# Performance work log

Measured on AMD Instinct MI355X. Metric: run time of the kernel, lower is better.

## Reference

```python
import jax, jax.numpy as jnp
import numpy as np

HIDDEN = 2048
HEADS = 16
HEAD_DIM = HIDDEN // HEADS
B, S = 4, 2048
NEG_INF = float('-inf')


def setup_inputs() -> dict:
    key = jax.random.key(0)
    ks = jax.random.split(key, 9)
    x = jax.random.normal(ks[0], (B, S, HIDDEN), dtype=jnp.float32)
    # causal mask: 0 on/below diagonal, -inf above (matches masked_fill(mask == -inf))
    causal = jnp.tril(jnp.ones((S, S), dtype=bool))
    mask = jnp.where(causal, 0.0, NEG_INF).astype(jnp.float32)[None, None]
    sc = 1.0 / np.sqrt(HIDDEN)
    Wq = jax.random.normal(ks[1], (HIDDEN, HIDDEN), jnp.float32) * sc
    Wk = jax.random.normal(ks[2], (HIDDEN, HIDDEN), jnp.float32) * sc
    Wv = jax.random.normal(ks[3], (HIDDEN, HIDDEN), jnp.float32) * sc
    Wo = jax.random.normal(ks[4], (HIDDEN, HIDDEN), jnp.float32) * sc
    bq = jax.random.normal(ks[5], (HIDDEN,), jnp.float32) * 0.02
    bk = jax.random.normal(ks[6], (HIDDEN,), jnp.float32) * 0.02
    bv = jax.random.normal(ks[7], (HIDDEN,), jnp.float32) * 0.02
    bo = jax.random.normal(ks[8], (HIDDEN,), jnp.float32) * 0.02
    return {"x": x, "mask": mask, "Wq": Wq, "bq": bq, "Wk": Wk, "bk": bk,
            "Wv": Wv, "bv": bv, "Wo": Wo, "bo": bo}


def reference(x, mask, Wq, bq, Wk, bk, Wv, bv, Wo, bo):
    Bsz, Slen, H = x.shape
    scale = jnp.float32(HEAD_DIM) ** 0.5
    # torch Linear: y = x @ W.T + b
    def proj(W, b):
        y = jnp.einsum('bsh,oh->bso', x, W) + b
        return y.reshape(Bsz, Slen, HEADS, HEAD_DIM).transpose(0, 2, 1, 3)  # [B,H,S,D]
    q = proj(Wq, bq)
    k = proj(Wk, bk)
    v = proj(Wv, bv)
    scores = jnp.einsum('bhqd,bhkd->bhqk', q, k) / scale
    scores = jnp.where(mask == NEG_INF, NEG_INF, scores)
    attn = jax.nn.softmax(scores, axis=-1)  # dropout is identity in eval
    ctx = jnp.einsum('bhqk,bhkd->bhqd', attn, v)
    ctx = ctx.transpose(0, 2, 1, 3).reshape(Bsz, Slen, H)
    return jnp.einsum('bsh,oh->bso', ctx, Wo) + bo
```

## Files before the change

### kernel.cpp

```cpp
#include <hip/hip_runtime.h>
#include <hip/hip_bf16.h>

#define HID 2048
#define NH 16
#define HD 128
#define SQ 2048
#define NB 4

typedef __attribute__((ext_vector_type(8))) short short8;
typedef __attribute__((ext_vector_type(4))) float f32x4;

__device__ __forceinline__ unsigned short f2bf(float f) {
  unsigned int u = __float_as_uint(f);
  u += 0x7fffu + ((u >> 16) & 1u);
  return (unsigned short)(u >> 16);
}
__device__ __forceinline__ unsigned int pkbf(float a, float b) {
  unsigned int ua = __float_as_uint(a) + 0x8000u;
  unsigned int ub = __float_as_uint(b) + 0x8000u;
  return (ua >> 16) | (ub & 0xffff0000u);
}
__device__ __forceinline__ f32x4 mfma16(short8 a, short8 b, f32x4 c) {
  return __builtin_amdgcn_mfma_f32_16x16x32_bf16(a, b, c, 0, 0, 0);
}
__device__ __forceinline__ void dma16(const void* g, void* l) {
  __builtin_amdgcn_global_load_lds(
      (__attribute__((address_space(1))) void*)(uintptr_t)g,
      (__attribute__((address_space(3))) void*)(uintptr_t)l, 16, 0, 0);
}
__device__ __forceinline__ void wgbar() {
  asm volatile("" ::: "memory");
  __builtin_amdgcn_s_barrier();
  asm volatile("" ::: "memory");
}

__global__ __launch_bounds__(256)
void cvt_bf16(const float* __restrict__ X, const float* __restrict__ Wq,
              const float* __restrict__ Wk, const float* __restrict__ Wv,
              const float* __restrict__ Wo, unsigned short* __restrict__ xbf,
              unsigned short* __restrict__ wbf)
{
  const size_t i8 = ((size_t)blockIdx.x * 256 + threadIdx.x) * 8;
  const float* src; unsigned short* dst; size_t off;
  const size_t XEL = (size_t)NB * SQ * HID;
  if (i8 < XEL) { src = X; dst = xbf; off = i8; }
  else {
    size_t t = i8 - XEL;
    int wi = (int)(t >> 22);
    off = t & ((1u << 22) - 1);
    src = (wi == 0) ? Wq : (wi == 1) ? Wk : (wi == 2) ? Wv : Wo;
    dst = wbf + ((size_t)wi << 22);
  }
  f32x4 a = *(const f32x4*)(src + off);
  f32x4 b = *(const f32x4*)(src + off + 4);
  short8 o;
  o[0] = (short)f2bf(a[0]); o[1] = (short)f2bf(a[1]);
  o[2] = (short)f2bf(a[2]); o[3] = (short)f2bf(a[3]);
  o[4] = (short)f2bf(b[0]); o[5] = (short)f2bf(b[1]);
  o[6] = (short)f2bf(b[2]); o[7] = (short)f2bf(b[3]);
  *(short8*)(dst + off) = o;
}

__global__ __launch_bounds__(512, 2)
void proj_gemm(const unsigned short* __restrict__ xbf,
               const unsigned short* __restrict__ wbf,
               const float* __restrict__ bq, const float* __restrict__ bk,
               const float* __restrict__ bv,
               unsigned short* __restrict__ qo, unsigned short* __restrict__ ko,
               unsigned short* __restrict__ vto)
{
  __shared__ unsigned short As[2][2][256 * 32];
  __shared__ unsigned short Bs[2][2][256 * 32];

  const int L = blockIdx.x;
  const int xcd = L & 7, sidx = L >> 3;
  const int mode = sidx >> 5;
  const int r5 = sidx & 31;
  const int mt = xcd * 4 + (r5 & 3);
  const int nt = r5 >> 2;
  const int m0 = mt * 256, n0 = nt * 256;

  const unsigned short* W = wbf + (size_t)mode * (HID * HID);
  const float* bias = (mode == 0) ? bq : (mode == 1) ? bk : bv;

  const int tid = threadIdx.x, lane = tid & 63, wv = tid >> 6;
  const int wm = wv >> 2, wn = wv & 3;
  const int g = lane >> 4, ln = lane & 15;

  const int srow = tid >> 2, scg = (tid & 3) ^ ((tid >> 3) & 3);
  const unsigned short* Ag = xbf + (size_t)(m0 + srow) * HID + scg * 8;
  const unsigned short* Bg = W + (size_t)(n0 + srow) * HID + scg * 8;

  f32x4 acc[8][4];
#pragma unroll
  for (int i = 0; i < 8; ++i)
#pragma unroll
    for (int j = 0; j < 4; ++j) acc[i][j] = (f32x4){0.f, 0.f, 0.f, 0.f};

  const int c8 = (g ^ ((ln >> 1) & 3)) * 8;
  const int arow0 = (wm * 128 + ln) * 32 + c8;
  const int brow0 = (wn * 64 + ln) * 32 + c8;

  auto stA = [&](int bufs, int khs, int kts) {
    const unsigned short* src = Ag + kts * 64 + khs * 32;
#pragma unroll
    for (int rr = 0; rr < 2; ++rr)
      dma16(src + (size_t)(rr * 128) * HID, &As[bufs][khs][rr * 4096 + wv * 512]);
  };
  auto stB = [&](int bufs, int khs, int kts) {
    const unsigned short* src = Bg + kts * 64 + khs * 32;
#pragma unroll
    for (int rr = 0; rr < 2; ++rr)
      dma16(src + (size_t)(rr * 128) * HID, &Bs[bufs][khs][rr * 4096 + wv * 512]);
  };

  stA(0, 0, 0); stB(0, 0, 0);
  stA(0, 1, 0); stB(0, 1, 0);
  stA(1, 0, 1); stB(1, 0, 1);
  asm volatile("s_waitcnt vmcnt(8)" ::: "memory");
  wgbar();

  for (int it = 0; it < 16; ++it) {
#pragma unroll
    for (int pp = 0; pp < 4; ++pp) {
      const int buf = (pp >> 1) & 1, khs = pp & 1;
      short8 af[8], bfr[4];
      const unsigned short* Ab = &As[buf][khs][0];
      const unsigned short* Bb = &Bs[buf][khs][0];
#pragma unroll
      for (int ii = 0; ii < 8; ++ii)
        af[ii] = *(const short8*)&Ab[arow0 + ii * 512];
#pragma unroll
      for (int j = 0; j < 4; ++j)
        bfr[j] = *(const short8*)&Bb[brow0 + j * 512];
      {
        const int kts = 2 * it + ((pp + 3) >> 1);
        if (kts < 32) {
          const int bufs = ((pp + 3) >> 1) & 1, khs_s = (pp + 3) & 1;
          stA(bufs, khs_s, kts); stB(bufs, khs_s, kts);
        }
      }
      asm volatile("s_waitcnt lgkmcnt(0)" ::: "memory");
      if (it == 15 && pp == 1)      asm volatile("s_waitcnt vmcnt(4)" ::: "memory");
      else if (it == 15 && pp >= 2) asm volatile("s_waitcnt vmcnt(0)" ::: "memory");
      else                          asm volatile("s_waitcnt vmcnt(8)" ::: "memory");
      wgbar();
      __builtin_amdgcn_sched_barrier(0);
      __builtin_amdgcn_s_setprio(1);
#pragma unroll
      for (int ii = 0; ii < 8; ++ii)
#pragma unroll
        for (int j = 0; j < 4; ++j)
          acc[ii][j] = mfma16(af[ii], bfr[j], acc[ii][j]);
      __builtin_amdgcn_s_setprio(0);
    }
  }

#pragma unroll
  for (int j = 0; j < 4; ++j) {
    const int ng = n0 + wn * 64 + j * 16 + ln;
    const float bb = bias[ng];
    const int h = ng >> 7, d = ng & (HD - 1);
#pragma unroll
    for (int i = 0; i < 8; ++i) {
      const int mg = m0 + wm * 128 + i * 16 + g * 4;
      const int b = mg >> 11, s0 = mg & (SQ - 1);
      if (mode == 2) {
        uint2 o2;
        o2.x = pkbf(acc[i][j][0] + bb, acc[i][j][1] + bb);
        o2.y = pkbf(acc[i][j][2] + bb, acc[i][j][3] + bb);
        *(uint2*)&vto[((size_t)(b * NH + h) * HD + d) * SQ + s0] = o2;
      } else {
        unsigned short* dst = (mode == 1) ? ko : qo;
#pragma unroll
        for (int r = 0; r < 4; ++r)
          dst[((size_t)(b * NH + h) * SQ + (s0 + r)) * HD + d] = f2bf(acc[i][j][r] + bb);
      }
    }
  }
}

__global__ __launch_bounds__(512, 2)
void attn(unsigned short* __restrict__ qc,
          const unsigned short* __restrict__ k,
          const unsigned short* __restrict__ vt)
{
  __shared__ unsigned short Ks[3][64 * 128];
  __shared__ unsigned short Vs[3][128 * 64];
  __shared__ unsigned short Ps[8][32 * 72];

  const int L = blockIdx.x;
  const int bh = L & 63;
  const int pr = L >> 6;
  const int tid = threadIdx.x, lane = tid & 63, w = tid >> 6;
  const int g = lane >> 4, ln = lane & 15;
  const float kScale = 0.12753102543f;

  const int krow = w * 4 + (lane >> 4);
  const int kchunk = lane & 15;
  const int vrow = w * 8 + (lane >> 3);
  const int vchunk = lane & 7;

  auto stK = [&](int buf, int t) {
#pragma unroll
    for (int i = 0; i < 2; ++i) {
      const int r = i * 32 + krow;
      dma16(k + ((size_t)bh * SQ + t * 64 + r) * HD + ((kchunk ^ (r & 15)) * 8),
            &Ks[buf][(i * 32 + w * 4) * 128]);
    }
  };
  auto stV = [&](int buf, int t) {
#pragma unroll
    for (int i = 0; i < 2; ++i) {
      const int r = i * 64 + vrow;
      dma16(vt + ((size_t)bh * HD + r) * SQ + t * 64 + ((vchunk ^ (r & 7)) * 8),
            &Vs[buf][(i * 64 + w * 8) * 64]);
    }
  };

  for (int ph = 0; ph < 2; ++ph) {
    const int qt = ph ? pr : 7 - pr;
    if (ph) wgbar();

    short8 qf[2][4];
    const size_t qrow = (size_t)bh * SQ + qt * 256 + w * 32;
#pragma unroll
    for (int n = 0; n < 2; ++n)
#pragma unroll
      for (int ks = 0; ks < 4; ++ks)
        qf[n][ks] = *(const short8*)(qc + (qrow + n * 16 + ln) * HD + ks * 32 + g * 8);
    asm volatile("" :: "v"(qf[0][0]), "v"(qf[0][1]), "v"(qf[0][2]), "v"(qf[0][3]),
                      "v"(qf[1][0]), "v"(qf[1][1]), "v"(qf[1][2]), "v"(qf[1][3]));

    f32x4 oacc[8][2];
    float lsum[2] = {0.f, 0.f};
#pragma unroll
    for (int jd = 0; jd < 8; ++jd)
#pragma unroll
      for (int n = 0; n < 2; ++n) oacc[jd][n] = (f32x4){0.f, 0.f, 0.f, 0.f};

    const int T = 4 * (qt + 1);
    stK(0, 0); stV(0, 0);
    stK(1, 1); stV(1, 1);

    int cur = 0;
    for (int t = 0; t < T; ++t) {
      if (t + 1 < T) asm volatile("s_waitcnt vmcnt(4)" ::: "memory");
      else           asm volatile("s_waitcnt vmcnt(0)" ::: "memory");
      wgbar();
      if (t + 2 < T) {
        int nb = cur + 2; if (nb >= 3) nb -= 3;
        stK(nb, t + 2); stV(nb, t + 2);
      }

      const int dqrel = qt * 256 + w * 32 - t * 64;
      if (dqrel + 31 >= 0) {
        int jm = ((dqrel + 31) >> 4) + 1; if (jm > 4) jm = 4;
        const bool masked = (dqrel < 63);

        f32x4 sacc[4][2];
#pragma unroll
        for (int j = 0; j < 4; ++j)
#pragma unroll
          for (int n = 0; n < 2; ++n) sacc[j][n] = (f32x4){0.f, 0.f, 0.f, 0.f};
        __builtin_amdgcn_s_setprio(1);
#pragma unroll
        for (int ks = 0; ks < 4; ++ks)
#pragma unroll
          for (int j = 0; j < 4; ++j)
            if (j < jm) {
              short8 kf = *(const short8*)&Ks[cur][(j * 16 + ln) * 128 + (((ks * 4 + g) ^ ln) * 8)];
              sacc[j][0] = mfma16(kf, qf[0][ks], sacc[j][0]);
              sacc[j][1] = mfma16(kf, qf[1][ks], sacc[j][1]);
            }
        __builtin_amdgcn_s_setprio(0);

#pragma unroll
        for (int j = 0; j < 4; ++j) {
          const int km = j * 16 + g * 4;
#pragma unroll
          for (int n = 0; n < 2; ++n) {
            f32x4 s4 = sacc[j][n];
            float e0 = exp2f(s4[0] * kScale);
            float e1 = exp2f(s4[1] * kScale);
            float e2 = exp2f(s4[2] * kScale);
            float e3 = exp2f(s4[3] * kScale);
            if (masked) {
              const int qm = dqrel + n * 16 + ln;
              if (km + 0 > qm) e0 = 0.f;
              if (km + 1 > qm) e1 = 0.f;
              if (km + 2 > qm) e2 = 0.f;
              if (km + 3 > qm) e3 = 0.f;
            }
            lsum[n] += (e0 + e1) + (e2 + e3);
            uint2 p2; p2.x = pkbf(e0, e1); p2.y = pkbf(e2, e3);
            *(uint2*)&Ps[w][(n * 16 + ln) * 72 + j * 16 + g * 4] = p2;
          }
        }

        short8 pa00 = *(const short8*)&Ps[w][ln * 72 + g * 8];
        short8 pa10 = *(const short8*)&Ps[w][(16 + ln) * 72 + g * 8];
        short8 pa01 = *(const short8*)&Ps[w][ln * 72 + 32 + g * 8];
        short8 pa11 = *(const short8*)&Ps[w][(16 + ln) * 72 + 32 + g * 8];
        const bool hi = (jm > 2);
        __builtin_amdgcn_s_setprio(1);
#pragma unroll
        for (int jd = 0; jd < 8; ++jd) {
          short8 vfa = *(const short8*)&Vs[cur][(jd * 16 + ln) * 64 + ((g ^ (ln & 7)) * 8)];
          oacc[jd][0] = mfma16(vfa, pa00, oacc[jd][0]);
          oacc[jd][1] = mfma16(vfa, pa10, oacc[jd][1]);
          if (hi) {
            short8 vfb = *(const short8*)&Vs[cur][(jd * 16 + ln) * 64 + (((4 + g) ^ (ln & 7)) * 8)];
            oacc[jd][0] = mfma16(vfb, pa01, oacc[jd][0]);
            oacc[jd][1] = mfma16(vfb, pa11, oacc[jd][1]);
          }
        }
        __builtin_amdgcn_s_setprio(0);
      }
      cur = (cur == 2) ? 0 : cur + 1;
    }

#pragma unroll
    for (int n = 0; n < 2; ++n) {
      float l = lsum[n];
      l += __shfl_xor(l, 16);
      l += __shfl_xor(l, 32);
      const float inv = 1.f / l;
      unsigned short* orow = qc + (qrow + n * 16 + ln) * HD;
#pragma unroll
      for (int jd = 0; jd < 8; ++jd) {
        uint2 o2;
        o2.x = pkbf(oacc[jd][n][0] * inv, oacc[jd][n][1] * inv);
        o2.y = pkbf(oacc[jd][n][2] * inv, oacc[jd][n][3] * inv);
        *(uint2*)(orow + jd * 16 + g * 4) = o2;
      }
    }
  }
}

__global__ __launch_bounds__(512, 2)
void out_gemm(const unsigned short* __restrict__ qc,
              const unsigned short* __restrict__ wobf,
              const float* __restrict__ bo, float* __restrict__ out)
{
  __shared__ unsigned short As[2][2][256 * 32];
  __shared__ unsigned short Bs[2][2][256 * 32];

  const int L = blockIdx.x;
  const int xcd = L & 7, r5 = L >> 3;
  const int mt = xcd * 4 + (r5 & 3);
  const int nt = r5 >> 2;
  const int m0 = mt * 256, n0 = nt * 256;

  const int tid = threadIdx.x, lane = tid & 63, wv = tid >> 6;
  const int wm = wv >> 2, wn = wv & 3;
  const int g = lane >> 4, ln = lane & 15;

  const int srow = tid >> 2, scg = (tid & 3) ^ ((tid >> 3) & 3);
  const int bI16 = (m0 >> 11) * 16;
  const int sbase = (m0 & (SQ - 1)) + srow;
  const unsigned short* Bg = wobf + (size_t)(n0 + srow) * HID + scg * 8;

  f32x4 acc[8][4];
#pragma unroll
  for (int i = 0; i < 8; ++i)
#pragma unroll
    for (int j = 0; j < 4; ++j) acc[i][j] = (f32x4){0.f, 0.f, 0.f, 0.f};

  const int c8 = (g ^ ((ln >> 1) & 3)) * 8;
  const int arow0 = (wm * 128 + ln) * 32 + c8;
  const int brow0 = (wn * 64 + ln) * 32 + c8;

  auto stA = [&](int bufs, int khs, int kts) {
    const unsigned short* src = qc + ((size_t)(bI16 + (kts >> 1)) * SQ + sbase) * HD
                                + (kts & 1) * 64 + khs * 32 + scg * 8;
#pragma unroll
    for (int rr = 0; rr < 2; ++rr)
      dma16(src + (size_t)(rr * 128) * HD, &As[bufs][khs][rr * 4096 + wv * 512]);
  };
  auto stB = [&](int bufs, int khs, int kts) {
    const unsigned short* src = Bg + kts * 64 + khs * 32;
#pragma unroll
    for (int rr = 0; rr < 2; ++rr)
      dma16(src + (size_t)(rr * 128) * HID, &Bs[bufs][khs][rr * 4096 + wv * 512]);
  };

  stA(0, 0, 0); stB(0, 0, 0);
  stA(0, 1, 0); stB(0, 1, 0);
  stA(1, 0, 1); stB(1, 0, 1);
  asm volatile("s_waitcnt vmcnt(8)" ::: "memory");
  wgbar();

  for (int it = 0; it < 16; ++it) {
#pragma unroll
    for (int pp = 0; pp < 4; ++pp) {
      const int buf = (pp >> 1) & 1, khs = pp & 1;
      short8 af[8], bfr[4];
      const unsigned short* Ab = &As[buf][khs][0];
      const unsigned short* Bb = &Bs[buf][khs][0];
#pragma unroll
      for (int ii = 0; ii < 8; ++ii)
        af[ii] = *(const short8*)&Ab[arow0 + ii * 512];
#pragma unroll
      for (int j = 0; j < 4; ++j)
        bfr[j] = *(const short8*)&Bb[brow0 + j * 512];
      {
        const int kts = 2 * it + ((pp + 3) >> 1);
        if (kts < 32) {
          const int bufs = ((pp + 3) >> 1) & 1, khs_s = (pp + 3) & 1;
          stA(bufs, khs_s, kts); stB(bufs, khs_s, kts);
        }
      }
      asm volatile("s_waitcnt lgkmcnt(0)" ::: "memory");
      if (it == 15 && pp == 1)      asm volatile("s_waitcnt vmcnt(4)" ::: "memory");
      else if (it == 15 && pp >= 2) asm volatile("s_waitcnt vmcnt(0)" ::: "memory");
      else                          asm volatile("s_waitcnt vmcnt(8)" ::: "memory");
      wgbar();
      __builtin_amdgcn_sched_barrier(0);
      __builtin_amdgcn_s_setprio(1);
#pragma unroll
      for (int ii = 0; ii < 8; ++ii)
#pragma unroll
        for (int j = 0; j < 4; ++j)
          acc[ii][j] = mfma16(af[ii], bfr[j], acc[ii][j]);
      __builtin_amdgcn_s_setprio(0);
    }
  }

#pragma unroll
  for (int j = 0; j < 4; ++j) {
    const int ng = n0 + wn * 64 + j * 16 + ln;
    const float bb = bo[ng];
#pragma unroll
    for (int i = 0; i < 8; ++i) {
      const int mg = m0 + wm * 128 + i * 16 + g * 4;
#pragma unroll
      for (int r = 0; r < 4; ++r)
        out[(size_t)(mg + r) * HID + ng] = acc[i][j][r] + bb;
    }
  }
}

extern "C" void kernel_launch(void* const* d_in, const int* in_sizes, int n_in,
                              void* d_out, int out_size, void* d_ws, size_t ws_size,
                              hipStream_t stream) {
  const float* x  = (const float*)d_in[0];
  const float* Wq = (const float*)d_in[2];
  const float* bq = (const float*)d_in[3];
  const float* Wk = (const float*)d_in[4];
  const float* bk = (const float*)d_in[5];
  const float* Wv = (const float*)d_in[6];
  const float* bv = (const float*)d_in[7];
  const float* Wo = (const float*)d_in[8];
  const float* bo = (const float*)d_in[9];
  float* out = (float*)d_out;

  const size_t WEL = (size_t)HID * HID;
  const size_t PER = (size_t)NB * NH * SQ * HD;
  unsigned short* wbf = (unsigned short*)d_ws;
  unsigned short* qw  = wbf + 4 * WEL;
  unsigned short* kw  = qw + PER;
  unsigned short* vtw = kw + PER;
  unsigned short* xbf = (unsigned short*)d_out;

  cvt_bf16<<<16384, 256, 0, stream>>>(x, Wq, Wk, Wv, Wo, xbf, wbf);

  proj_gemm<<<768, 512, 0, stream>>>(xbf, wbf, bq, bk, bv, qw, kw, vtw);

  attn<<<256, 512, 0, stream>>>(qw, kw, vtw);

  out_gemm<<<256, 512, 0, stream>>>(qw, wbf + 3 * WEL, bo, out);
}
```

Measured before the change: 567.0 us.

## Restructure causal attention: one q-tile per block, register P shuffle, double buffering

The attention kernel now launches 512 blocks, each handling one 256-row query tile, instead of 256 blocks that each paired a long and a short tile. Blocks are mapped so the longest causal tiles get scheduled first and heads are spread across XCDs. The P matrix is redistributed between lanes with cross-lane shuffles instead of a round trip through LDS. K/V staging drops from triple to double buffering, which shrinks LDS so up to four blocks can fit per CU. The cost is that each K/V load is now fully exposed by the vmcnt(0) wait before every tile, plus extra shuffle instructions, and load balance now depends on the hardware scheduler rather than explicit tile pairing.

New measurement: 998.5 us. +76.1%, slower.

```diff
diff --git a/kernel.cpp b/kernel.cpp
--- a/kernel.cpp
+++ b/kernel.cpp
@@ -9,6 +9,7 @@
 
 typedef __attribute__((ext_vector_type(8))) short short8;
 typedef __attribute__((ext_vector_type(4))) float f32x4;
+typedef __attribute__((ext_vector_type(4))) unsigned int u32x4;
 
 __device__ __forceinline__ unsigned short f2bf(float f) {
   unsigned int u = __float_as_uint(f);
@@ -180,18 +181,18 @@
   }
 }
 
-__global__ __launch_bounds__(512, 2)
+__global__ __launch_bounds__(512, 4)
 void attn(unsigned short* __restrict__ qc,
           const unsigned short* __restrict__ k,
           const unsigned short* __restrict__ vt)
 {
-  __shared__ unsigned short Ks[3][64 * 128];
-  __shared__ unsigned short Vs[3][128 * 64];
-  __shared__ unsigned short Ps[8][32 * 72];
+  __shared__ unsigned short Ks[2][64 * 128];
+  __shared__ unsigned short Vs[2][128 * 64];
 
   const int L = blockIdx.x;
-  const int bh = L & 63;
-  const int pr = L >> 6;
+  const int xcd = L & 7;
+  const int qt = 7 - ((L >> 3) & 7);
+  const int bh = xcd + 8 * (L >> 6);
   const int tid = threadIdx.x, lane = tid & 63, w = tid >> 6;
   const int g = lane >> 4, ln = lane & 15;
   const float kScale = 0.12753102543f;
@@ -218,122 +219,133 @@
     }
   };
 
-  for (int ph = 0; ph < 2; ++ph) {
-    const int qt = ph ? pr : 7 - pr;
-    if (ph) wgbar();
-
-    short8 qf[2][4];
-    const size_t qrow = (size_t)bh * SQ + qt * 256 + w * 32;
-#pragma unroll
-    for (int n = 0; n < 2; ++n)
-#pragma unroll
-      for (int ks = 0; ks < 4; ++ks)
-        qf[n][ks] = *(const short8*)(qc + (qrow + n * 16 + ln) * HD + ks * 32 + g * 8);
-    asm volatile("" :: "v"(qf[0][0]), "v"(qf[0][1]), "v"(qf[0][2]), "v"(qf[0][3]),
-                      "v"(qf[1][0]), "v"(qf[1][1]), "v"(qf[1][2]), "v"(qf[1][3]));
-
-    f32x4 oacc[8][2];
-    float lsum[2] = {0.f, 0.f};
-#pragma unroll
-    for (int jd = 0; jd < 8; ++jd)
-#pragma unroll
-      for (int n = 0; n < 2; ++n) oacc[jd][n] = (f32x4){0.f, 0.f, 0.f, 0.f};
-
-    const int T = 4 * (qt + 1);
-    stK(0, 0); stV(0, 0);
-    stK(1, 1); stV(1, 1);
-
-    int cur = 0;
-    for (int t = 0; t < T; ++t) {
-      if (t + 1 < T) asm volatile("s_waitcnt vmcnt(4)" ::: "memory");
-      else           asm volatile("s_waitcnt vmcnt(0)" ::: "memory");
-      wgbar();
-      if (t + 2 < T) {
-        int nb = cur + 2; if (nb >= 3) nb -= 3;
-        stK(nb, t + 2); stV(nb, t + 2);
-      }
-
-      const int dqrel = qt * 256 + w * 32 - t * 64;
-      if (dqrel + 31 >= 0) {
-        int jm = ((dqrel + 31) >> 4) + 1; if (jm > 4) jm = 4;
-        const bool masked = (dqrel < 63);
-
-        f32x4 sacc[4][2];
-#pragma unroll
-        for (int j = 0; j < 4; ++j)
-#pragma unroll
-          for (int n = 0; n < 2; ++n) sacc[j][n] = (f32x4){0.f, 0.f, 0.f, 0.f};
-        __builtin_amdgcn_s_setprio(1);
-#pragma unroll
-        for (int ks = 0; ks < 4; ++ks)
-#pragma unroll
-          for (int j = 0; j < 4; ++j)
-            if (j < jm) {
-              short8 kf = *(const short8*)&Ks[cur][(j * 16 + ln) * 128 + (((ks * 4 + g) ^ ln) * 8)];
-              sacc[j][0] = mfma16(kf, qf[0][ks], sacc[j][0]);
-              sacc[j][1] = mfma16(kf, qf[1][ks], sacc[j][1]);
-            }
-        __builtin_amdgcn_s_setprio(0);
-
-#pragma unroll
-        for (int j = 0; j < 4; ++j) {
-          const int km = j * 16 + g * 4;
-#pragma unroll
-          for (int n = 0; n < 2; ++n) {
-            f32x4 s4 = sacc[j][n];
-            float e0 = exp2f(s4[0] * kScale);
-            float e1 = exp2f(s4[1] * kScale);
-            float e2 = exp2f(s4[2] * kScale);
-            float e3 = exp2f(s4[3] * kScale);
-            if (masked) {
-              const int qm = dqrel + n * 16 + ln;
-              if (km + 0 > qm) e0 = 0.f;
-              if (km + 1 > qm) e1 = 0.f;
-              if (km + 2 > qm) e2 = 0.f;
-              if (km + 3 > qm) e3 = 0.f;
-            }
-            lsum[n] += (e0 + e1) + (e2 + e3);
-            uint2 p2; p2.x = pkbf(e0, e1); p2.y = pkbf(e2, e3);
-            *(uint2*)&Ps[w][(n * 16 + ln) * 72 + j * 16 + g * 4] = p2;
+  short8 qf[2][4];
+  const size_t qrow = (size_t)bh * SQ + qt * 256 + w * 32;
+#pragma unroll
+  for (int n = 0; n < 2; ++n)
+#pragma unroll
+    for (int ks = 0; ks < 4; ++ks)
+      qf[n][ks] = *(const short8*)(qc + (qrow + n * 16 + ln) * HD + ks * 32 + g * 8);
+  asm volatile("" :: "v"(qf[0][0]), "v"(qf[0][1]), "v"(qf[0][2]), "v"(qf[0][3]),
+                    "v"(qf[1][0]), "v"(qf[1][1]), "v"(qf[1][2]), "v"(qf[1][3]));
+
+  f32x4 oacc[8][2];
+  float lsum[2] = {0.f, 0.f};
+#pragma unroll
+  for (int jd = 0; jd < 8; ++jd)
+#pragma unroll
+    for (int n = 0; n < 2; ++n) oacc[jd][n] = (f32x4){0.f, 0.f, 0.f, 0.f};
+
+  const int T = 4 * (qt + 1);
+  stK(0, 0); stV(0, 0);
+
+  const int src0 = ((g & 1) << 5) + ln;
+  const int src1 = src0 + 16;
+  const bool jh = (g >= 2);
+
+  for (int t = 0; t < T; ++t) {
+    const int cur = t & 1;
+    asm volatile("s_waitcnt vmcnt(0)" ::: "memory");
+    wgbar();
+    if (t + 1 < T) { stK(cur ^ 1, t + 1); stV(cur ^ 1, t + 1); }
+
+    const int dqrel = qt * 256 + w * 32 - t * 64;
+    if (dqrel + 31 >= 0) {
+      int jm = ((dqrel + 31) >> 4) + 1; if (jm > 4) jm = 4;
+      const bool masked = (dqrel < 63);
+
+      unsigned int pk[2][4][2];
+#pragma unroll
+      for (int j = 0; j < 4; ++j) {
+        f32x4 s0 = (f32x4){0.f, 0.f, 0.f, 0.f};
+        f32x4 s1 = (f32x4){0.f, 0.f, 0.f, 0.f};
+        if (j < jm) {
+          __builtin_amdgcn_s_setprio(1);
+#pragma unroll
+          for (int ks = 0; ks < 4; ++ks) {
+            short8 kf = *(const short8*)&Ks[cur][(j * 16 + ln) * 128 + (((ks * 4 + g) ^ ln) * 8)];
+            s0 = mfma16(kf, qf[0][ks], s0);
+            s1 = mfma16(kf, qf[1][ks], s1);
           }
-        }
-
-        short8 pa00 = *(const short8*)&Ps[w][ln * 72 + g * 8];
-        short8 pa10 = *(const short8*)&Ps[w][(16 + ln) * 72 + g * 8];
-        short8 pa01 = *(const short8*)&Ps[w][ln * 72 + 32 + g * 8];
-        short8 pa11 = *(const short8*)&Ps[w][(16 + ln) * 72 + 32 + g * 8];
-        const bool hi = (jm > 2);
-        __builtin_amdgcn_s_setprio(1);
-#pragma unroll
-        for (int jd = 0; jd < 8; ++jd) {
-          short8 vfa = *(const short8*)&Vs[cur][(jd * 16 + ln) * 64 + ((g ^ (ln & 7)) * 8)];
-          oacc[jd][0] = mfma16(vfa, pa00, oacc[jd][0]);
-          oacc[jd][1] = mfma16(vfa, pa10, oacc[jd][1]);
-          if (hi) {
-            short8 vfb = *(const short8*)&Vs[cur][(jd * 16 + ln) * 64 + (((4 + g) ^ (ln & 7)) * 8)];
-            oacc[jd][0] = mfma16(vfb, pa01, oacc[jd][0]);
-            oacc[jd][1] = mfma16(vfb, pa11, oacc[jd][1]);
+          __builtin_amdgcn_s_setprio(0);
+        }
+        const int km = j * 16 + g * 4;
+#pragma unroll
+        for (int n = 0; n < 2; ++n) {
+          f32x4 s4 = (n == 0) ? s0 : s1;
+          float e0 = exp2f(s4[0] * kScale);
+          float e1 = exp2f(s4[1] * kScale);
+          float e2 = exp2f(s4[2] * kScale);
+          float e3 = exp2f(s4[3] * kScale);
+          if (masked) {
+            const int qm = dqrel + n * 16 + ln;
+            if (km + 0 > qm) e0 = 0.f;
+            if (km + 1 > qm) e1 = 0.f;
+            if (km + 2 > qm) e2 = 0.f;
+            if (km + 3 > qm) e3 = 0.f;
           }
-        }
-        __builtin_amdgcn_s_setprio(0);
-      }
-      cur = (cur == 2) ? 0 : cur + 1;
-    }
-
-#pragma unroll
-    for (int n = 0; n < 2; ++n) {
-      float l = lsum[n];
-      l += __shfl_xor(l, 16);
-      l += __shfl_xor(l, 32);
-      const float inv = 1.f / l;
-      unsigned short* orow = qc + (qrow + n * 16 + ln) * HD;
+          lsum[n] += (e0 + e1) + (e2 + e3);
+          pk[n][j][0] = pkbf(e0, e1);
+          pk[n][j][1] = pkbf(e2, e3);
+        }
+      }
+
+      short8 pa0[2], pa1[2];
+#pragma unroll
+      for (int n = 0; n < 2; ++n) {
+        unsigned int va[4], vb[4];
+#pragma unroll
+        for (int i = 0; i < 2; ++i) {
+          unsigned int t0 = (unsigned int)__shfl((int)pk[n][0][i], src0);
+          unsigned int t1 = (unsigned int)__shfl((int)pk[n][1][i], src0);
+          va[i] = jh ? t1 : t0;
+          unsigned int t2 = (unsigned int)__shfl((int)pk[n][0][i], src1);
+          unsigned int t3 = (unsigned int)__shfl((int)pk[n][1][i], src1);
+          va[2 + i] = jh ? t3 : t2;
+          unsigned int u0 = (unsigned int)__shfl((int)pk[n][2][i], src0);
+          unsigned int u1 = (unsigned int)__shfl((int)pk[n][3][i], src0);
+          vb[i] = jh ? u1 : u0;
+          unsigned int u2 = (unsigned int)__shfl((int)pk[n][2][i], src1);
+          unsigned int u3 = (unsigned int)__shfl((int)pk[n][3][i], src1);
+          vb[2 + i] = jh ? u3 : u2;
+        }
+        union { u32x4 u; short8 s; } ca, cb;
+        ca.u = (u32x4){va[0], va[1], va[2], va[3]};
+        cb.u = (u32x4){vb[0], vb[1], vb[2], vb[3]};
+        pa0[n] = ca.s;
+        pa1[n] = cb.s;
+      }
+
+      const bool hi = (jm > 2);
+      __builtin_amdgcn_s_setprio(1);
 #pragma unroll
       for (int jd = 0; jd < 8; ++jd) {
-        uint2 o2;
-        o2.x = pkbf(oacc[jd][n][0] * inv, oacc[jd][n][1] * inv);
-        o2.y = pkbf(oacc[jd][n][2] * inv, oacc[jd][n][3] * inv);
-        *(uint2*)(orow + jd * 16 + g * 4) = o2;
-      }
+        short8 vfa = *(const short8*)&Vs[cur][(jd * 16 + ln) * 64 + ((g ^ (ln & 7)) * 8)];
+        oacc[jd][0] = mfma16(vfa, pa0[0], oacc[jd][0]);
+        oacc[jd][1] = mfma16(vfa, pa0[1], oacc[jd][1]);
+        if (hi) {
+          short8 vfb = *(const short8*)&Vs[cur][(jd * 16 + ln) * 64 + (((4 + g) ^ (ln & 7)) * 8)];
+          oacc[jd][0] = mfma16(vfb, pa1[0], oacc[jd][0]);
+          oacc[jd][1] = mfma16(vfb, pa1[1], oacc[jd][1]);
+        }
+      }
+      __builtin_amdgcn_s_setprio(0);
+    }
+  }
+
+#pragma unroll
+  for (int n = 0; n < 2; ++n) {
+    float l = lsum[n];
+    l += __shfl_xor(l, 16);
+    l += __shfl_xor(l, 32);
+    const float inv = 1.f / l;
+    unsigned short* orow = qc + (qrow + n * 16 + ln) * HD;
+#pragma unroll
+    for (int jd = 0; jd < 8; ++jd) {
+      uint2 o2;
+      o2.x = pkbf(oacc[jd][n][0] * inv, oacc[jd][n][1] * inv);
+      o2.y = pkbf(oacc[jd][n][2] * inv, oacc[jd][n][3] * inv);
+      *(uint2*)(orow + jd * 16 + g * 4) = o2;
     }
   }
 }
@@ -467,7 +479,7 @@
 
   proj_gemm<<<768, 512, 0, stream>>>(xbf, wbf, bq, bk, bv, qw, kw, vtw);
 
-  attn<<<256, 512, 0, stream>>>(qw, kw, vtw);
+  attn<<<512, 512, 0, stream>>>(qw, kw, vtw);
 
   out_gemm<<<256, 512, 0, stream>>>(qw, wbf + 3 * WEL, bo, out);
 }
```
